# Performance work log

Measured on AMD Instinct MI355X. Metric: run time of the kernel, lower is better.

Reference implementation:

```python
import jax, jax.numpy as jnp
import numpy as np

B, LQ, LKV, D, DV = 8, 2048, 2048, 128, 128


def setup_inputs() -> dict:
    key = jax.random.key(0)
    kq, kk, kv = jax.random.split(key, 3)
    return {
        "query": jax.random.normal(kq, (B, LQ, D), dtype=jnp.float32),
        "key": jax.random.normal(kk, (B, LKV, D), dtype=jnp.float32),
        "value": jax.random.normal(kv, (B, LKV, DV), dtype=jnp.float32),
    }


def reference(query, key, value):
    # score_fn: scaled dot-product  score = Q K^T / sqrt(Dq)
    scale = 1.0 / jnp.sqrt(jnp.asarray(query.shape[-1], query.dtype))
    score = jnp.einsum("bqd,bkd->bqk", query, key) * scale  # (B, Lq, Lkv)
    attention_weights = jax.nn.softmax(score, axis=-1)
    context_vector = jnp.einsum("bqk,bkv->bqv", attention_weights, value)
    return attention_weights, context_vector
```

## Files before the change

### kernel.cpp

```cpp
#include <hip/hip_runtime.h>

#define BB    8
#define LQN   2048
#define LKVN  2048
#define DQ    128
#define DVN   128
#define QT    16
#define KT    64
#define KSTR  136
#define VSTR  72
#define PSTR  72
#define NT    (LKVN / KT)

typedef short short8 __attribute__((ext_vector_type(8)));
typedef float f32x4  __attribute__((ext_vector_type(4)));

__device__ __forceinline__ short f2bf(float f) {
  unsigned u = __builtin_bit_cast(unsigned, f);
  u += 0x7fffu + ((u >> 16) & 1u);
  return (short)(u >> 16);
}

__global__ __launch_bounds__(256) void conv_kernel(const float* __restrict__ Q,
                                                   const float* __restrict__ K,
                                                   short* __restrict__ Qb,
                                                   short* __restrict__ Kb) {
  int i = blockIdx.x * 256 + threadIdx.x;
  const float* s; short* d;
  if (i < 262144) { s = Q; d = Qb; }
  else            { s = K; d = Kb; i -= 262144; }
  size_t off = (size_t)i * 8;
  float4 a = *(const float4*)(s + off);
  float4 b = *(const float4*)(s + off + 4);
  short8 o;
  o[0] = f2bf(a.x); o[1] = f2bf(a.y); o[2] = f2bf(a.z); o[3] = f2bf(a.w);
  o[4] = f2bf(b.x); o[5] = f2bf(b.y); o[6] = f2bf(b.z); o[7] = f2bf(b.w);
  *(short8*)(d + off) = o;
}

__global__ __launch_bounds__(256) void vtrans_kernel(const float* __restrict__ V,
                                                     short* __restrict__ Vt) {
  __shared__ float tile[128][33];
  const int kv0 = blockIdx.x * 128;
  const int dv0 = blockIdx.y * 32;
  const int b   = blockIdx.z;
  const int tid = threadIdx.x;
  const float* src = V + ((size_t)b * LKVN + kv0) * DVN + dv0;
#pragma unroll
  for (int it = 0; it < 4; ++it) {
    int idx = it * 256 + tid;
    int r = idx >> 3, c4 = idx & 7;
    float4 v = *(const float4*)(src + (size_t)r * DVN + c4 * 4);
    tile[r][c4 * 4 + 0] = v.x;
    tile[r][c4 * 4 + 1] = v.y;
    tile[r][c4 * 4 + 2] = v.z;
    tile[r][c4 * 4 + 3] = v.w;
  }
  __syncthreads();
  short* dst = Vt + ((size_t)b * DVN + dv0) * LKVN + kv0;
#pragma unroll
  for (int it = 0; it < 2; ++it) {
    int idx = it * 256 + tid;
    int row = idx >> 4, ch = idx & 15;
    short8 o;
#pragma unroll
    for (int j = 0; j < 8; ++j) o[j] = f2bf(tile[ch * 8 + j][row]);
    *(short8*)(dst + (size_t)row * LKVN + ch * 8) = o;
  }
}

__global__ __launch_bounds__(256, 4) void attn_kernel(const short* __restrict__ Qb,
                                                      const short* __restrict__ Kb,
                                                      const short* __restrict__ Vt,
                                                      float* __restrict__ W,
                                                      float* __restrict__ O) {
  __shared__ __align__(16) short k_lds[KT][KSTR];
  __shared__ __align__(16) short v_lds[DVN][VSTR];
  __shared__ __align__(16) short p_lds[QT][PSTR];
  __shared__ float red_l[4][QT];
  __shared__ float stats_r[QT];

  const int tid  = threadIdx.x;
  const int w    = tid >> 6;
  const int lane = tid & 63;
  const int n    = lane & 15;
  const int qd   = lane >> 4;
  const int b    = blockIdx.x & 7;
  const int q0   = (blockIdx.x >> 3) * QT;

  const short* Kbase = Kb + (size_t)b * LKVN * DQ;
  const short* Vbase = Vt + (size_t)b * DVN * LKVN;

  const int kr = tid >> 4, kc = tid & 15;
  const int vr = tid >> 3, vc = tid & 7;

  short8 qf[4];
  {
    const short* Qrow = Qb + ((size_t)b * LQN + q0 + n) * DQ + qd * 8;
#pragma unroll
    for (int ks = 0; ks < 4; ++ks) qf[ks] = *(const short8*)(Qrow + ks * 32);
  }

  const float scale = 0.08838834764831845f;
  float l_part[4] = {0.f, 0.f, 0.f, 0.f};
  short8 kreg[4], vreg[4];

#pragma unroll
  for (int it = 0; it < 4; ++it)
    kreg[it] = *(const short8*)(Kbase + (size_t)(kr + it * 16) * DQ + kc * 8);
#pragma unroll
  for (int it = 0; it < 4; ++it)
    *(short8*)&k_lds[kr + it * 16][kc * 8] = kreg[it];

  for (int t = 0; t < NT; ++t) {
    __syncthreads();
    if (t + 1 < NT) {
      const short* src = Kbase + (size_t)(t + 1) * KT * DQ;
#pragma unroll
      for (int it = 0; it < 4; ++it)
        kreg[it] = *(const short8*)(src + (size_t)(kr + it * 16) * DQ + kc * 8);
    }
    f32x4 acc = {0.f, 0.f, 0.f, 0.f};
#pragma unroll
    for (int ks = 0; ks < 4; ++ks) {
      short8 bf = *(const short8*)&k_lds[w * 16 + n][ks * 32 + qd * 8];
      acc = __builtin_amdgcn_mfma_f32_16x16x32_bf16(qf[ks], bf, acc, 0, 0, 0);
    }
#pragma unroll
    for (int r = 0; r < 4; ++r) l_part[r] += __expf(acc[r] * scale);
    __syncthreads();
    if (t + 1 < NT) {
#pragma unroll
      for (int it = 0; it < 4; ++it)
        *(short8*)&k_lds[kr + it * 16][kc * 8] = kreg[it];
    }
  }

#pragma unroll
  for (int r = 0; r < 4; ++r)
#pragma unroll
    for (int off = 1; off < 16; off <<= 1)
      l_part[r] += __shfl_xor(l_part[r], off, 64);
  if (n == 0)
#pragma unroll
    for (int r = 0; r < 4; ++r) red_l[w][qd * 4 + r] = l_part[r];
  __syncthreads();
  if (tid < QT)
    stats_r[tid] = 1.0f / (red_l[0][tid] + red_l[1][tid] + red_l[2][tid] + red_l[3][tid]);
  __syncthreads();
  float rinv[4];
#pragma unroll
  for (int r = 0; r < 4; ++r) rinv[r] = stats_r[qd * 4 + r];

  f32x4 oacc[2];
  oacc[0] = (f32x4){0.f, 0.f, 0.f, 0.f};
  oacc[1] = (f32x4){0.f, 0.f, 0.f, 0.f};
  float* Wb = W + ((size_t)b * LQN + q0) * LKVN;

#pragma unroll
  for (int it = 0; it < 4; ++it)
    kreg[it] = *(const short8*)(Kbase + (size_t)(kr + it * 16) * DQ + kc * 8);
#pragma unroll
  for (int it = 0; it < 4; ++it)
    vreg[it] = *(const short8*)(Vbase + (size_t)(vr + it * 32) * LKVN + vc * 8);
#pragma unroll
  for (int it = 0; it < 4; ++it)
    *(short8*)&k_lds[kr + it * 16][kc * 8] = kreg[it];
#pragma unroll
  for (int it = 0; it < 4; ++it)
    *(short8*)&v_lds[vr + it * 32][vc * 8] = vreg[it];

  for (int t = 0; t < NT; ++t) {
    const int kv0 = t * KT;
    __syncthreads();
    if (t + 1 < NT) {
      const short* ksrc = Kbase + (size_t)(kv0 + KT) * DQ;
      const short* vsrc = Vbase + kv0 + KT;
#pragma unroll
      for (int it = 0; it < 4; ++it)
        kreg[it] = *(const short8*)(ksrc + (size_t)(kr + it * 16) * DQ + kc * 8);
#pragma unroll
      for (int it = 0; it < 4; ++it)
        vreg[it] = *(const short8*)(vsrc + (size_t)(vr + it * 32) * LKVN + vc * 8);
    }
    f32x4 acc = {0.f, 0.f, 0.f, 0.f};
#pragma unroll
    for (int ks = 0; ks < 4; ++ks) {
      short8 bf = *(const short8*)&k_lds[w * 16 + n][ks * 32 + qd * 8];
      acc = __builtin_amdgcn_mfma_f32_16x16x32_bf16(qf[ks], bf, acc, 0, 0, 0);
    }
    float p[4];
#pragma unroll
    for (int r = 0; r < 4; ++r) p[r] = __expf(acc[r] * scale) * rinv[r];
#pragma unroll
    for (int r = 0; r < 4; ++r)
      Wb[(size_t)(qd * 4 + r) * LKVN + kv0 + w * 16 + n] = p[r];
#pragma unroll
    for (int r = 0; r < 4; ++r) p_lds[qd * 4 + r][w * 16 + n] = f2bf(p[r]);
    __syncthreads();
    short8 pa0 = *(const short8*)&p_lds[n][qd * 8];
    short8 pa1 = *(const short8*)&p_lds[n][32 + qd * 8];
#pragma unroll
    for (int c = 0; c < 2; ++c) {
      const int dv = w * 32 + c * 16 + n;
      short8 b0 = *(const short8*)&v_lds[dv][qd * 8];
      short8 b1 = *(const short8*)&v_lds[dv][32 + qd * 8];
      oacc[c] = __builtin_amdgcn_mfma_f32_16x16x32_bf16(pa0, b0, oacc[c], 0, 0, 0);
      oacc[c] = __builtin_amdgcn_mfma_f32_16x16x32_bf16(pa1, b1, oacc[c], 0, 0, 0);
    }
    __syncthreads();
    if (t + 1 < NT) {
#pragma unroll
      for (int it = 0; it < 4; ++it)
        *(short8*)&k_lds[kr + it * 16][kc * 8] = kreg[it];
#pragma unroll
      for (int it = 0; it < 4; ++it)
        *(short8*)&v_lds[vr + it * 32][vc * 8] = vreg[it];
    }
  }

  float* Ob = O + ((size_t)b * LQN + q0) * DVN;
#pragma unroll
  for (int c = 0; c < 2; ++c)
#pragma unroll
    for (int r = 0; r < 4; ++r)
      Ob[(size_t)(qd * 4 + r) * DVN + w * 32 + c * 16 + n] = oacc[c][r];
}

extern "C" void kernel_launch(void* const* d_in, const int* in_sizes, int n_in,
                              void* d_out, int out_size, void* d_ws, size_t ws_size,
                              hipStream_t stream) {
  const float* Q = (const float*)d_in[0];
  const float* K = (const float*)d_in[1];
  const float* V = (const float*)d_in[2];
  float* W = (float*)d_out;
  float* O = W + (size_t)BB * LQN * LKVN;
  short* Qb = (short*)d_ws;
  short* Kb = Qb + (size_t)BB * LQN * DQ;
  short* Vt = Kb + (size_t)BB * LKVN * DQ;

  conv_kernel<<<2048, 256, 0, stream>>>(Q, K, Qb, Kb);
  vtrans_kernel<<<dim3(LKVN / 128, DVN / 32, BB), 256, 0, stream>>>(V, Vt);
  attn_kernel<<<1024, 256, 0, stream>>>(Qb, Kb, Vt, W, O);
}
```

Before: 224.6 us.

## Restructure attention LDS pipeline: load fragments early, double-buffer P, fewer barriers

The normalization pass now uses 128-row K tiles, so it runs half as many iterations. Each iteration reads the K fragments into registers and then issues a single barrier before refilling LDS. The weights pass likewise reads K and V fragments into registers up front, double-buffers the P tile by iteration parity, and writes the next K/V tile before one mid-iteration barrier, which cuts per-iteration barriers from three to two. The two passes share one manually carved LDS buffer to keep the footprint small. The cost is a custom asm barrier that only waits on lgkmcnt, plus more registers live per thread.

```diff
diff --git a/kernel.cpp b/kernel.cpp
--- a/kernel.cpp
+++ b/kernel.cpp
@@ -7,13 +7,17 @@
 #define DVN   128
 #define QT    16
 #define KT    64
+#define KT1   128
+#define NT    (LKVN / KT)
+#define NT1   (LKVN / KT1)
 #define KSTR  136
 #define VSTR  72
 #define PSTR  72
-#define NT    (LKVN / KT)
 
 typedef short short8 __attribute__((ext_vector_type(8)));
 typedef float f32x4  __attribute__((ext_vector_type(4)));
+
+#define BAR() asm volatile("s_waitcnt lgkmcnt(0)\n\ts_barrier" ::: "memory")
 
 __device__ __forceinline__ short f2bf(float f) {
   unsigned u = __builtin_bit_cast(unsigned, f);
@@ -69,16 +73,20 @@
   }
 }
 
+#define SMEM_BYTES 40768
+
 __global__ __launch_bounds__(256, 4) void attn_kernel(const short* __restrict__ Qb,
                                                       const short* __restrict__ Kb,
                                                       const short* __restrict__ Vt,
                                                       float* __restrict__ W,
                                                       float* __restrict__ O) {
-  __shared__ __align__(16) short k_lds[KT][KSTR];
-  __shared__ __align__(16) short v_lds[DVN][VSTR];
-  __shared__ __align__(16) short p_lds[QT][PSTR];
-  __shared__ float red_l[4][QT];
-  __shared__ float stats_r[QT];
+  __shared__ __align__(16) char smem[SMEM_BYTES];
+  short (*k1)[KSTR] = (short(*)[KSTR])smem;
+  short (*k2)[KSTR] = (short(*)[KSTR])smem;
+  short (*vl)[VSTR] = (short(*)[VSTR])(smem + 17408);
+  short (*pl)[QT][PSTR] = (short(*)[QT][PSTR])(smem + 35840);
+  float (*redl)[QT] = (float(*)[QT])(smem + 40448);
+  float* statr = (float*)(smem + 40704);
 
   const int tid  = threadIdx.x;
   const int w    = tid >> 6;
@@ -103,36 +111,46 @@
 
   const float scale = 0.08838834764831845f;
   float l_part[4] = {0.f, 0.f, 0.f, 0.f};
-  short8 kreg[4], vreg[4];
-
-#pragma unroll
-  for (int it = 0; it < 4; ++it)
-    kreg[it] = *(const short8*)(Kbase + (size_t)(kr + it * 16) * DQ + kc * 8);
-#pragma unroll
-  for (int it = 0; it < 4; ++it)
-    *(short8*)&k_lds[kr + it * 16][kc * 8] = kreg[it];
-
-  for (int t = 0; t < NT; ++t) {
-    __syncthreads();
-    if (t + 1 < NT) {
-      const short* src = Kbase + (size_t)(t + 1) * KT * DQ;
-#pragma unroll
-      for (int it = 0; it < 4; ++it)
-        kreg[it] = *(const short8*)(src + (size_t)(kr + it * 16) * DQ + kc * 8);
-    }
-    f32x4 acc = {0.f, 0.f, 0.f, 0.f};
-#pragma unroll
-    for (int ks = 0; ks < 4; ++ks) {
-      short8 bf = *(const short8*)&k_lds[w * 16 + n][ks * 32 + qd * 8];
-      acc = __builtin_amdgcn_mfma_f32_16x16x32_bf16(qf[ks], bf, acc, 0, 0, 0);
-    }
-#pragma unroll
-    for (int r = 0; r < 4; ++r) l_part[r] += __expf(acc[r] * scale);
-    __syncthreads();
-    if (t + 1 < NT) {
-#pragma unroll
-      for (int it = 0; it < 4; ++it)
-        *(short8*)&k_lds[kr + it * 16][kc * 8] = kreg[it];
+
+  {
+    short8 kreg[8];
+#pragma unroll
+    for (int it = 0; it < 8; ++it)
+      kreg[it] = *(const short8*)(Kbase + (size_t)(kr + it * 16) * DQ + kc * 8);
+#pragma unroll
+    for (int it = 0; it < 8; ++it)
+      *(short8*)&k1[kr + it * 16][kc * 8] = kreg[it];
+    BAR();
+
+    for (int t = 0; t < NT1; ++t) {
+      short8 bf[2][4];
+#pragma unroll
+      for (int c = 0; c < 2; ++c)
+#pragma unroll
+        for (int ks = 0; ks < 4; ++ks)
+          bf[c][ks] = *(const short8*)&k1[c * 64 + w * 16 + n][ks * 32 + qd * 8];
+      BAR();
+      if (t + 1 < NT1) {
+        const short* src = Kbase + (size_t)(t + 1) * KT1 * DQ;
+#pragma unroll
+        for (int it = 0; it < 8; ++it)
+          kreg[it] = *(const short8*)(src + (size_t)(kr + it * 16) * DQ + kc * 8);
+      }
+      f32x4 a0 = {0.f, 0.f, 0.f, 0.f}, a1 = {0.f, 0.f, 0.f, 0.f};
+#pragma unroll
+      for (int ks = 0; ks < 4; ++ks) {
+        a0 = __builtin_amdgcn_mfma_f32_16x16x32_bf16(qf[ks], bf[0][ks], a0, 0, 0, 0);
+        a1 = __builtin_amdgcn_mfma_f32_16x16x32_bf16(qf[ks], bf[1][ks], a1, 0, 0, 0);
+      }
+#pragma unroll
+      for (int r = 0; r < 4; ++r)
+        l_part[r] += __expf(a0[r] * scale) + __expf(a1[r] * scale);
+      if (t + 1 < NT1) {
+#pragma unroll
+        for (int it = 0; it < 8; ++it)
+          *(short8*)&k1[kr + it * 16][kc * 8] = kreg[it];
+      }
+      BAR();
     }
   }
 
@@ -143,20 +161,21 @@
       l_part[r] += __shfl_xor(l_part[r], off, 64);
   if (n == 0)
 #pragma unroll
-    for (int r = 0; r < 4; ++r) red_l[w][qd * 4 + r] = l_part[r];
+    for (int r = 0; r < 4; ++r) redl[w][qd * 4 + r] = l_part[r];
   __syncthreads();
   if (tid < QT)
-    stats_r[tid] = 1.0f / (red_l[0][tid] + red_l[1][tid] + red_l[2][tid] + red_l[3][tid]);
+    statr[tid] = 1.0f / (redl[0][tid] + redl[1][tid] + redl[2][tid] + redl[3][tid]);
   __syncthreads();
   float rinv[4];
 #pragma unroll
-  for (int r = 0; r < 4; ++r) rinv[r] = stats_r[qd * 4 + r];
+  for (int r = 0; r < 4; ++r) rinv[r] = statr[qd * 4 + r];
 
   f32x4 oacc[2];
   oacc[0] = (f32x4){0.f, 0.f, 0.f, 0.f};
   oacc[1] = (f32x4){0.f, 0.f, 0.f, 0.f};
   float* Wb = W + ((size_t)b * LQN + q0) * LKVN;
 
+  short8 kreg[4], vreg[4];
 #pragma unroll
   for (int it = 0; it < 4; ++it)
     kreg[it] = *(const short8*)(Kbase + (size_t)(kr + it * 16) * DQ + kc * 8);
@@ -165,14 +184,24 @@
     vreg[it] = *(const short8*)(Vbase + (size_t)(vr + it * 32) * LKVN + vc * 8);
 #pragma unroll
   for (int it = 0; it < 4; ++it)
-    *(short8*)&k_lds[kr + it * 16][kc * 8] = kreg[it];
-#pragma unroll
-  for (int it = 0; it < 4; ++it)
-    *(short8*)&v_lds[vr + it * 32][vc * 8] = vreg[it];
+    *(short8*)&k2[kr + it * 16][kc * 8] = kreg[it];
+#pragma unroll
+  for (int it = 0; it < 4; ++it)
+    *(short8*)&vl[vr + it * 32][vc * 8] = vreg[it];
+  BAR();
 
   for (int t = 0; t < NT; ++t) {
     const int kv0 = t * KT;
-    __syncthreads();
+    short8 bf[4], vf[2][2];
+#pragma unroll
+    for (int ks = 0; ks < 4; ++ks)
+      bf[ks] = *(const short8*)&k2[w * 16 + n][ks * 32 + qd * 8];
+#pragma unroll
+    for (int c = 0; c < 2; ++c) {
+      vf[c][0] = *(const short8*)&vl[w * 32 + c * 16 + n][qd * 8];
+      vf[c][1] = *(const short8*)&vl[w * 32 + c * 16 + n][32 + qd * 8];
+    }
+    BAR();
     if (t + 1 < NT) {
       const short* ksrc = Kbase + (size_t)(kv0 + KT) * DQ;
       const short* vsrc = Vbase + kv0 + KT;
@@ -185,10 +214,8 @@
     }
     f32x4 acc = {0.f, 0.f, 0.f, 0.f};
 #pragma unroll
-    for (int ks = 0; ks < 4; ++ks) {
-      short8 bf = *(const short8*)&k_lds[w * 16 + n][ks * 32 + qd * 8];
-      acc = __builtin_amdgcn_mfma_f32_16x16x32_bf16(qf[ks], bf, acc, 0, 0, 0);
-    }
+    for (int ks = 0; ks < 4; ++ks)
+      acc = __builtin_amdgcn_mfma_f32_16x16x32_bf16(qf[ks], bf[ks], acc, 0, 0, 0);
     float p[4];
 #pragma unroll
     for (int r = 0; r < 4; ++r) p[r] = __expf(acc[r] * scale) * rinv[r];
@@ -196,26 +223,22 @@
     for (int r = 0; r < 4; ++r)
       Wb[(size_t)(qd * 4 + r) * LKVN + kv0 + w * 16 + n] = p[r];
 #pragma unroll
-    for (int r = 0; r < 4; ++r) p_lds[qd * 4 + r][w * 16 + n] = f2bf(p[r]);
-    __syncthreads();
-    short8 pa0 = *(const short8*)&p_lds[n][qd * 8];
-    short8 pa1 = *(const short8*)&p_lds[n][32 + qd * 8];
+    for (int r = 0; r < 4; ++r) pl[t & 1][qd * 4 + r][w * 16 + n] = f2bf(p[r]);
+    if (t + 1 < NT) {
+#pragma unroll
+      for (int it = 0; it < 4; ++it)
+        *(short8*)&k2[kr + it * 16][kc * 8] = kreg[it];
+#pragma unroll
+      for (int it = 0; it < 4; ++it)
+        *(short8*)&vl[vr + it * 32][vc * 8] = vreg[it];
+    }
+    BAR();
+    short8 pa0 = *(const short8*)&pl[t & 1][n][qd * 8];
+    short8 pa1 = *(const short8*)&pl[t & 1][n][32 + qd * 8];
 #pragma unroll
     for (int c = 0; c < 2; ++c) {
-      const int dv = w * 32 + c * 16 + n;
-      short8 b0 = *(const short8*)&v_lds[dv][qd * 8];
-      short8 b1 = *(const short8*)&v_lds[dv][32 + qd * 8];
-      oacc[c] = __builtin_amdgcn_mfma_f32_16x16x32_bf16(pa0, b0, oacc[c], 0, 0, 0);
-      oacc[c] = __builtin_amdgcn_mfma_f32_16x16x32_bf16(pa1, b1, oacc[c], 0, 0, 0);
-    }
-    __syncthreads();
-    if (t + 1 < NT) {
-#pragma unroll
-      for (int it = 0; it < 4; ++it)
-        *(short8*)&k_lds[kr + it * 16][kc * 8] = kreg[it];
-#pragma unroll
-      for (int it = 0; it < 4; ++it)
-        *(short8*)&v_lds[vr + it * 32][vc * 8] = vreg[it];
+      oacc[c] = __builtin_amdgcn_mfma_f32_16x16x32_bf16(pa0, vf[c][0], oacc[c], 0, 0, 0);
+      oacc[c] = __builtin_amdgcn_mfma_f32_16x16x32_bf16(pa1, vf[c][1], oacc[c], 0, 0, 0);
     }
   }
 
```

Result: slower. 237.1 us (+5.6%).

## Load K/V fragments directly from global into registers, stage W writes via LDS

Applied to the files above, without the earlier changes.

Drops the LDS staging of K and V tiles. Each wave now loads its MFMA operand fragments straight from global memory into double-buffered registers, which removes most barriers. The W output is staged through a double-buffered LDS tile so each thread writes float4 rows for coalesced stores, and exp is computed as exp2 with a prescaled constant. A single barrier per iteration with double-buffered P/W LDS replaces three syncthreads. The cost is more global and L2 traffic for K/V, since fragments are no longer shared across waves through LDS, plus higher register pressure.

```diff
diff --git a/kernel.cpp b/kernel.cpp
--- a/kernel.cpp
+++ b/kernel.cpp
@@ -7,13 +7,14 @@
 #define DVN   128
 #define QT    16
 #define KT    64
-#define KSTR  136
-#define VSTR  72
+#define NT    (LKVN / KT)
 #define PSTR  72
-#define NT    (LKVN / KT)
+#define WSTR  68
 
 typedef short short8 __attribute__((ext_vector_type(8)));
 typedef float f32x4  __attribute__((ext_vector_type(4)));
+
+#define BAR() asm volatile("s_waitcnt lgkmcnt(0)\n\ts_barrier" ::: "memory")
 
 __device__ __forceinline__ short f2bf(float f) {
   unsigned u = __builtin_bit_cast(unsigned, f);
@@ -74,11 +75,10 @@
                                                       const short* __restrict__ Vt,
                                                       float* __restrict__ W,
                                                       float* __restrict__ O) {
-  __shared__ __align__(16) short k_lds[KT][KSTR];
-  __shared__ __align__(16) short v_lds[DVN][VSTR];
-  __shared__ __align__(16) short p_lds[QT][PSTR];
-  __shared__ float red_l[4][QT];
-  __shared__ float stats_r[QT];
+  __shared__ __align__(16) short pl[2][QT][PSTR];
+  __shared__ __align__(16) float pw[2][QT][WSTR];
+  __shared__ float redl[4][QT];
+  __shared__ float statr[QT];
 
   const int tid  = threadIdx.x;
   const int w    = tid >> 6;
@@ -91,9 +91,6 @@
   const short* Kbase = Kb + (size_t)b * LKVN * DQ;
   const short* Vbase = Vt + (size_t)b * DVN * LKVN;
 
-  const int kr = tid >> 4, kc = tid & 15;
-  const int vr = tid >> 3, vc = tid & 7;
-
   short8 qf[4];
   {
     const short* Qrow = Qb + ((size_t)b * LQN + q0 + n) * DQ + qd * 8;
@@ -101,38 +98,28 @@
     for (int ks = 0; ks < 4; ++ks) qf[ks] = *(const short8*)(Qrow + ks * 32);
   }
 
-  const float scale = 0.08838834764831845f;
+  const float k2c = (float)(0.08838834764831845 * 1.4426950408889634);
   float l_part[4] = {0.f, 0.f, 0.f, 0.f};
-  short8 kreg[4], vreg[4];
-
-#pragma unroll
-  for (int it = 0; it < 4; ++it)
-    kreg[it] = *(const short8*)(Kbase + (size_t)(kr + it * 16) * DQ + kc * 8);
-#pragma unroll
-  for (int it = 0; it < 4; ++it)
-    *(short8*)&k_lds[kr + it * 16][kc * 8] = kreg[it];
-
-  for (int t = 0; t < NT; ++t) {
-    __syncthreads();
-    if (t + 1 < NT) {
-      const short* src = Kbase + (size_t)(t + 1) * KT * DQ;
-#pragma unroll
-      for (int it = 0; it < 4; ++it)
-        kreg[it] = *(const short8*)(src + (size_t)(kr + it * 16) * DQ + kc * 8);
-    }
-    f32x4 acc = {0.f, 0.f, 0.f, 0.f};
-#pragma unroll
-    for (int ks = 0; ks < 4; ++ks) {
-      short8 bf = *(const short8*)&k_lds[w * 16 + n][ks * 32 + qd * 8];
-      acc = __builtin_amdgcn_mfma_f32_16x16x32_bf16(qf[ks], bf, acc, 0, 0, 0);
-    }
-#pragma unroll
-    for (int r = 0; r < 4; ++r) l_part[r] += __expf(acc[r] * scale);
-    __syncthreads();
-    if (t + 1 < NT) {
-#pragma unroll
-      for (int it = 0; it < 4; ++it)
-        *(short8*)&k_lds[kr + it * 16][kc * 8] = kreg[it];
+
+  {
+    const short* Kp = Kbase + ((size_t)(w * 32 * 16 + n)) * DQ + qd * 8;
+    short8 kb[2][4];
+#pragma unroll
+    for (int ks = 0; ks < 4; ++ks) kb[0][ks] = *(const short8*)(Kp + ks * 32);
+#pragma unroll 2
+    for (int i = 0; i < 32; ++i) {
+      const int cur = i & 1, nxt = cur ^ 1;
+      if (i + 1 < 32) {
+        const short* src = Kp + (size_t)(i + 1) * 16 * DQ;
+#pragma unroll
+        for (int ks = 0; ks < 4; ++ks) kb[nxt][ks] = *(const short8*)(src + ks * 32);
+      }
+      f32x4 acc = {0.f, 0.f, 0.f, 0.f};
+#pragma unroll
+      for (int ks = 0; ks < 4; ++ks)
+        acc = __builtin_amdgcn_mfma_f32_16x16x32_bf16(qf[ks], kb[cur][ks], acc, 0, 0, 0);
+#pragma unroll
+      for (int r = 0; r < 4; ++r) l_part[r] += exp2f(acc[r] * k2c);
     }
   }
 
@@ -143,80 +130,71 @@
       l_part[r] += __shfl_xor(l_part[r], off, 64);
   if (n == 0)
 #pragma unroll
-    for (int r = 0; r < 4; ++r) red_l[w][qd * 4 + r] = l_part[r];
+    for (int r = 0; r < 4; ++r) redl[w][qd * 4 + r] = l_part[r];
   __syncthreads();
   if (tid < QT)
-    stats_r[tid] = 1.0f / (red_l[0][tid] + red_l[1][tid] + red_l[2][tid] + red_l[3][tid]);
+    statr[tid] = 1.0f / (redl[0][tid] + redl[1][tid] + redl[2][tid] + redl[3][tid]);
   __syncthreads();
   float rinv[4];
 #pragma unroll
-  for (int r = 0; r < 4; ++r) rinv[r] = stats_r[qd * 4 + r];
+  for (int r = 0; r < 4; ++r) rinv[r] = statr[qd * 4 + r];
 
   f32x4 oacc[2];
   oacc[0] = (f32x4){0.f, 0.f, 0.f, 0.f};
   oacc[1] = (f32x4){0.f, 0.f, 0.f, 0.f};
   float* Wb = W + ((size_t)b * LQN + q0) * LKVN;
 
-#pragma unroll
-  for (int it = 0; it < 4; ++it)
-    kreg[it] = *(const short8*)(Kbase + (size_t)(kr + it * 16) * DQ + kc * 8);
-#pragma unroll
-  for (int it = 0; it < 4; ++it)
-    vreg[it] = *(const short8*)(Vbase + (size_t)(vr + it * 32) * LKVN + vc * 8);
-#pragma unroll
-  for (int it = 0; it < 4; ++it)
-    *(short8*)&k_lds[kr + it * 16][kc * 8] = kreg[it];
-#pragma unroll
-  for (int it = 0; it < 4; ++it)
-    *(short8*)&v_lds[vr + it * 32][vc * 8] = vreg[it];
-
+  const short* Kp2 = Kbase + ((size_t)(w * 16 + n)) * DQ + qd * 8;
+  const short* Vp2 = Vbase + ((size_t)(w * 32 + n)) * LKVN + qd * 8;
+  const int wrow = tid >> 4, wcol = (tid & 15) * 4;
+
+  short8 kfb[2][4], vfb[2][4];
+#pragma unroll
+  for (int ks = 0; ks < 4; ++ks) kfb[0][ks] = *(const short8*)(Kp2 + ks * 32);
+#pragma unroll
+  for (int c = 0; c < 2; ++c) {
+    vfb[0][c * 2 + 0] = *(const short8*)(Vp2 + (size_t)c * 16 * LKVN);
+    vfb[0][c * 2 + 1] = *(const short8*)(Vp2 + (size_t)c * 16 * LKVN + 32);
+  }
+
+#pragma unroll 2
   for (int t = 0; t < NT; ++t) {
     const int kv0 = t * KT;
-    __syncthreads();
+    const int cur = t & 1, nxt = cur ^ 1;
     if (t + 1 < NT) {
-      const short* ksrc = Kbase + (size_t)(kv0 + KT) * DQ;
-      const short* vsrc = Vbase + kv0 + KT;
-#pragma unroll
-      for (int it = 0; it < 4; ++it)
-        kreg[it] = *(const short8*)(ksrc + (size_t)(kr + it * 16) * DQ + kc * 8);
-#pragma unroll
-      for (int it = 0; it < 4; ++it)
-        vreg[it] = *(const short8*)(vsrc + (size_t)(vr + it * 32) * LKVN + vc * 8);
+      const short* ks2 = Kp2 + (size_t)(kv0 + KT) * DQ;
+      const short* vs2 = Vp2 + kv0 + KT;
+#pragma unroll
+      for (int ks = 0; ks < 4; ++ks) kfb[nxt][ks] = *(const short8*)(ks2 + ks * 32);
+#pragma unroll
+      for (int c = 0; c < 2; ++c) {
+        vfb[nxt][c * 2 + 0] = *(const short8*)(vs2 + (size_t)c * 16 * LKVN);
+        vfb[nxt][c * 2 + 1] = *(const short8*)(vs2 + (size_t)c * 16 * LKVN + 32);
+      }
     }
     f32x4 acc = {0.f, 0.f, 0.f, 0.f};
 #pragma unroll
-    for (int ks = 0; ks < 4; ++ks) {
-      short8 bf = *(const short8*)&k_lds[w * 16 + n][ks * 32 + qd * 8];
-      acc = __builtin_amdgcn_mfma_f32_16x16x32_bf16(qf[ks], bf, acc, 0, 0, 0);
-    }
+    for (int ks = 0; ks < 4; ++ks)
+      acc = __builtin_amdgcn_mfma_f32_16x16x32_bf16(qf[ks], kfb[cur][ks], acc, 0, 0, 0);
     float p[4];
 #pragma unroll
-    for (int r = 0; r < 4; ++r) p[r] = __expf(acc[r] * scale) * rinv[r];
-#pragma unroll
-    for (int r = 0; r < 4; ++r)
-      Wb[(size_t)(qd * 4 + r) * LKVN + kv0 + w * 16 + n] = p[r];
-#pragma unroll
-    for (int r = 0; r < 4; ++r) p_lds[qd * 4 + r][w * 16 + n] = f2bf(p[r]);
-    __syncthreads();
-    short8 pa0 = *(const short8*)&p_lds[n][qd * 8];
-    short8 pa1 = *(const short8*)&p_lds[n][32 + qd * 8];
-#pragma unroll
-    for (int c = 0; c < 2; ++c) {
-      const int dv = w * 32 + c * 16 + n;
-      short8 b0 = *(const short8*)&v_lds[dv][qd * 8];
-      short8 b1 = *(const short8*)&v_lds[dv][32 + qd * 8];
-      oacc[c] = __builtin_amdgcn_mfma_f32_16x16x32_bf16(pa0, b0, oacc[c], 0, 0, 0);
-      oacc[c] = __builtin_amdgcn_mfma_f32_16x16x32_bf16(pa1, b1, oacc[c], 0, 0, 0);
-    }
-    __syncthreads();
-    if (t + 1 < NT) {
-#pragma unroll
-      for (int it = 0; it < 4; ++it)
-        *(short8*)&k_lds[kr + it * 16][kc * 8] = kreg[it];
-#pragma unroll
-      for (int it = 0; it < 4; ++it)
-        *(short8*)&v_lds[vr + it * 32][vc * 8] = vreg[it];
-    }
+    for (int r = 0; r < 4; ++r) p[r] = exp2f(acc[r] * k2c) * rinv[r];
+#pragma unroll
+    for (int r = 0; r < 4; ++r) {
+      pw[cur][qd * 4 + r][w * 16 + n] = p[r];
+      pl[cur][qd * 4 + r][w * 16 + n] = f2bf(p[r]);
+    }
+    BAR();
+    {
+      float4 wv = *(const float4*)&pw[cur][wrow][wcol];
+      *(float4*)(Wb + (size_t)wrow * LKVN + kv0 + wcol) = wv;
+    }
+    short8 pa0 = *(const short8*)&pl[cur][n][qd * 8];
+    short8 pa1 = *(const short8*)&pl[cur][n][32 + qd * 8];
+    oacc[0] = __builtin_amdgcn_mfma_f32_16x16x32_bf16(pa0, vfb[cur][0], oacc[0], 0, 0, 0);
+    oacc[0] = __builtin_amdgcn_mfma_f32_16x16x32_bf16(pa1, vfb[cur][1], oacc[0], 0, 0, 0);
+    oacc[1] = __builtin_amdgcn_mfma_f32_16x16x32_bf16(pa0, vfb[cur][2], oacc[1], 0, 0, 0);
+    oacc[1] = __builtin_amdgcn_mfma_f32_16x16x32_bf16(pa1, vfb[cur][3], oacc[1], 0, 0, 0);
   }
 
   float* Ob = O + ((size_t)b * LQN + q0) * DVN;
```

Result: slower. 316.6 us (+41.0%).
